# Kernel optimization log

Measured on AMD Instinct MI355X. Metric: run time of the kernel, lower is better.

The kernel has to match this reference:

```python
import jax, jax.numpy as jnp
import numpy as np

N, E, D, H = 4096, 131072, 256, 8
DH = D // H  # head dim = 32


def layer_norm(x, g, b, eps=1e-5):
    mu = jnp.mean(x, axis=-1, keepdims=True)
    var = jnp.var(x, axis=-1, keepdims=True)
    return (x - mu) * jax.lax.rsqrt(var + eps) * g + b


def mlp2(x, w1, b1, w2, b2):
    # Linear -> GELU(exact) -> Linear (dropout is identity at inference)
    return jax.nn.gelu(x @ w1 + b1, approximate=False) @ w2 + b2


def setup_inputs() -> dict:
    key = jax.random.key(0)
    ks = iter(jax.random.split(key, 32))
    s = 0.02
    d = {
        'x': jax.random.normal(next(ks), (N, D), jnp.float32),
        'edge_index': jax.random.randint(next(ks), (2, E), 0, N, jnp.int32),
        'edge_attr': jax.random.normal(next(ks), (E, D), jnp.float32),
        # GINE eps
        'eps': jnp.zeros((1,), jnp.float32),
        # edge MLP (Linear weights stored [in, out])
        'e_w1': jax.random.normal(next(ks), (D, D), jnp.float32) * s,
        'e_b1': jnp.zeros((D,), jnp.float32),
        'e_w2': jax.random.normal(next(ks), (D, D), jnp.float32) * s,
        'e_b2': jnp.zeros((D,), jnp.float32),
        # update MLP
        'u_w1': jax.random.normal(next(ks), (D, D), jnp.float32) * s,
        'u_b1': jnp.zeros((D,), jnp.float32),
        'u_w2': jax.random.normal(next(ks), (D, D), jnp.float32) * s,
        'u_b2': jnp.zeros((D,), jnp.float32),
        # LayerNorms
        'ln_local_g': jnp.ones((D,), jnp.float32), 'ln_local_b': jnp.zeros((D,), jnp.float32),
        'ln_global_g': jnp.ones((D,), jnp.float32), 'ln_global_b': jnp.zeros((D,), jnp.float32),
        'ln_ffn_g': jnp.ones((D,), jnp.float32), 'ln_ffn_b': jnp.zeros((D,), jnp.float32),
        # MHA projections ([in, out])
        'wq': jax.random.normal(next(ks), (D, D), jnp.float32) * s,
        'wk': jax.random.normal(next(ks), (D, D), jnp.float32) * s,
        'wv': jax.random.normal(next(ks), (D, D), jnp.float32) * s,
        'bq': jnp.zeros((D,), jnp.float32), 'bk': jnp.zeros((D,), jnp.float32), 'bv': jnp.zeros((D,), jnp.float32),
        'wo': jax.random.normal(next(ks), (D, D), jnp.float32) * s,
        'bo': jnp.zeros((D,), jnp.float32),
        # FFN
        'f_w1': jax.random.normal(next(ks), (D, 4 * D), jnp.float32) * s,
        'f_b1': jnp.zeros((4 * D,), jnp.float32),
        'f_w2': jax.random.normal(next(ks), (4 * D, D), jnp.float32) * s,
        'f_b2': jnp.zeros((D,), jnp.float32),
    }
    return d


def reference(x, edge_index, edge_attr, eps,
              e_w1, e_b1, e_w2, e_b2, u_w1, u_b1, u_w2, u_b2,
              ln_local_g, ln_local_b, ln_global_g, ln_global_b, ln_ffn_g, ln_ffn_b,
              wq, wk, wv, bq, bk, bv, wo, bo,
              f_w1, f_b1, f_w2, f_b2):
    src, dst = edge_index[0], edge_index[1]
    n = x.shape[0]

    # ---- local GINE conv on pre-normed features ----
    h = layer_norm(x, ln_local_g, ln_local_b)
    messages = mlp2(h[src] + edge_attr, e_w1, e_b1, e_w2, e_b2)  # [E, D]
    aggregated = jax.ops.segment_sum(messages, dst, num_segments=n)  # [N, D]
    local = mlp2((1.0 + eps) * h + aggregated, u_w1, u_b1, u_w2, u_b2)
    x = x + local

    # ---- global multihead self-attention over all nodes ----
    g = layer_norm(x, ln_global_g, ln_global_b)
    q = (g @ wq + bq).reshape(n, H, DH)
    k = (g @ wk + bk).reshape(n, H, DH)
    v = (g @ wv + bv).reshape(n, H, DH)
    scores = jnp.einsum('nhd,mhd->hnm', q, k) / jnp.sqrt(jnp.float32(DH))
    attn = jax.nn.softmax(scores, axis=-1)
    ctx = jnp.einsum('hnm,mhd->nhd', attn, v).reshape(n, D)
    x = x + (ctx @ wo + bo)

    # ---- FFN ----
    x = x + mlp2(layer_norm(x, ln_ffn_g, ln_ffn_b), f_w1, f_b1, f_w2, f_b2)
    return x
```

## Files before the change

### kernel.cpp

```cpp
#include <hip/hip_runtime.h>
#include <math.h>

#define N_NODES 4096
#define N_EDGES 131072
#define XPAD    264

using bf16x8 = __attribute__((ext_vector_type(8))) __bf16;
using bf16x4 = __attribute__((ext_vector_type(4))) __bf16;
using f32x4  = __attribute__((ext_vector_type(4))) float;
typedef unsigned short u16;

__device__ __forceinline__ u16 f2bf(float f) {
  union { __bf16 b; u16 u; } cv; cv.b = (__bf16)f; return cv.u;
}
__device__ __forceinline__ float bf2f(u16 h) {
  return __uint_as_float(((unsigned)h) << 16);
}
__device__ __forceinline__ float gelu_tanh(float x) {
  float t = x * x;
  float y = x * (1.5957691216057308f + 0.07135481627f * t);
  float e = __expf(y);
  return x - x / (1.0f + e);
}
__device__ __forceinline__ f32x4 mfma16(bf16x8 a, bf16x8 b, f32x4 c) {
  return __builtin_amdgcn_mfma_f32_16x16x32_bf16(a, b, c, 0, 0, 0);
}

struct WPtrs { const float* p[10]; };

__global__ void setup_kernel(WPtrs w, u16* __restrict__ dst, float qscale,
                             const int* __restrict__ ei, int* __restrict__ deg,
                             const float* __restrict__ bq, const float* __restrict__ bk,
                             const float* __restrict__ bv, float* __restrict__ qkvbias) {
  int blk = blockIdx.x, t = threadIdx.x;
  if (blk < 512) {
    int tid = blk * 256 + t;
    int m, ci;
    if (tid < 32768)      { m = tid >> 13;                 ci = tid & 8191; }
    else if (tid < 57344) { m = 4 + ((tid - 32768) >> 13); ci = (tid - 32768) & 8191; }
    else if (tid < 65536) { m = 7; ci = tid - 57344; }
    else if (tid < 98304) { m = 8; ci = tid - 65536; }
    else                  { m = 9; ci = tid - 98304; }
    int Cols = (m == 8) ? 1024 : 256;
    int k8   = (m == 8) ? (ci >> 10) : (ci >> 8);
    int c    = (m == 8) ? (ci & 1023) : (ci & 255);
    const float* src = w.p[m] + (size_t)(k8 * 8) * Cols + c;
    float sc = (m == 4) ? qscale : 1.0f;
    u16 tmp[8];
#pragma unroll
    for (int j = 0; j < 8; ++j) tmp[j] = f2bf(src[(size_t)j * Cols] * sc);
    size_t off;
    if (m < 4)       off = (size_t)(m << 16) + (size_t)(k8 * 256 + c) * 8;
    else if (m < 7)  off = 262144 + (size_t)(k8 * 768 + (m - 4) * 256 + c) * 8;
    else if (m == 7) off = 458752 + (size_t)(k8 * 256 + c) * 8;
    else if (m == 8) off = 524288 + (size_t)(k8 * 1024 + c) * 8;
    else             off = 786432 + (size_t)(k8 * 256 + c) * 8;
    *(uint4*)(dst + off) = *(const uint4*)tmp;
  } else if (blk < 1024) {
    int e = (blk - 512) * 256 + t;
    atomicAdd(&deg[ei[N_EDGES + e]], 1);
  } else {
#pragma unroll
    for (int i = 0; i < 3; ++i) {
      int idx = i * 256 + t;
      qkvbias[idx] = idx < 256 ? bq[idx] * qscale : (idx < 512 ? bk[idx - 256] : bv[idx - 512]);
    }
  }
}

__global__ void scan_kernel(const int* __restrict__ deg, int* __restrict__ offs) {
  __shared__ int part[1024];
  int t = threadIdx.x;
  int base = t * 4;
  int a0 = deg[base], a1 = deg[base + 1], a2 = deg[base + 2], a3 = deg[base + 3];
  int s = a0 + a1 + a2 + a3;
  part[t] = s;
  __syncthreads();
  for (int off = 1; off < 1024; off <<= 1) {
    int v = (t >= off) ? part[t - off] : 0;
    __syncthreads();
    part[t] += v;
    __syncthreads();
  }
  int excl = part[t] - s;
  offs[base] = excl;
  offs[base + 1] = excl + a0;
  offs[base + 2] = excl + a0 + a1;
  offs[base + 3] = excl + a0 + a1 + a2;
  if (t == 1023) offs[4096] = part[1023];
}

__global__ void mid_kernel(const int* __restrict__ ei, const int* __restrict__ offs,
                           int* __restrict__ cnt, int* __restrict__ eperm,
                           int* __restrict__ dst_s, int* __restrict__ src_s,
                           const float* __restrict__ x, const float* __restrict__ g,
                           const float* __restrict__ b, float* __restrict__ hf,
                           u16* __restrict__ hb) {
  int blk = blockIdx.x, t = threadIdx.x;
  if (blk < 512) {
    int e = blk * 256 + t;
    int d = ei[N_EDGES + e];
    int p = offs[d] + atomicAdd(&cnt[d], 1);
    eperm[p] = e;
    dst_s[p] = d;
    src_s[p] = ei[e];
  } else {
    int row = blk - 512;
    float v = x[(size_t)row * 256 + t];
    float s1 = v, s2 = v * v;
#pragma unroll
    for (int o = 32; o > 0; o >>= 1) { s1 += __shfl_xor(s1, o); s2 += __shfl_xor(s2, o); }
    __shared__ float a1[4], a2[4];
    int wv = t >> 6, lane = t & 63;
    if (lane == 0) { a1[wv] = s1; a2[wv] = s2; }
    __syncthreads();
    s1 = a1[0] + a1[1] + a1[2] + a1[3];
    s2 = a2[0] + a2[1] + a2[2] + a2[3];
    float mean = s1 * (1.0f / 256.0f);
    float var  = s2 * (1.0f / 256.0f) - mean * mean;
    float rs = rsqrtf(var + 1e-5f);
    float o = (v - mean) * rs * g[t] + b[t];
    hf[(size_t)row * 256 + t] = o;
    hb[(size_t)row * 256 + t] = f2bf(o);
  }
}

__launch_bounds__(256, 2)
__global__ void edge_kernel(const u16* __restrict__ hb, const float* __restrict__ ea,
                            const int* __restrict__ eperm, const int* __restrict__ src_s,
                            const int* __restrict__ dst_s,
                            const u16* __restrict__ wp1, const float* __restrict__ b1,
                            const u16* __restrict__ wp2, const float* __restrict__ b2,
                            float* __restrict__ agg) {
  __shared__ __align__(16) u16 X[128 * XPAD];
  const f32x4 fzero = {0.f, 0.f, 0.f, 0.f};
  int t = threadIdx.x;
  int lane = t & 63, wv = t >> 6;
  int lr = lane & 15, lq = lane >> 4;
  int e0 = blockIdx.x * 128;
  int col0 = wv * 64;

  const u16* b1ptr = wp1 + ((size_t)lq * 256 + col0 + lr) * 8;
  const u16* b2ptr = wp2 + ((size_t)lq * 256 + col0 + lr) * 8;
  bf16x8 bc[4], bn[4];
#pragma unroll
  for (int ct = 0; ct < 4; ++ct) bc[ct] = *(const bf16x8*)(b1ptr + ct * 128);

  int ci = (t & 31) * 8;
#pragma unroll
  for (int it = 0; it < 16; ++it) {
    int r = it * 8 + (t >> 5);
    int e = eperm[e0 + r];
    int s = src_s[e0 + r];
    const float* pa = ea + (size_t)e * 256 + ci;
    float4 a0 = *(const float4*)pa;
    float4 a1 = *(const float4*)(pa + 4);
    ushort4 h0 = *(const ushort4*)(hb + (size_t)s * 256 + ci);
    ushort4 h1 = *(const ushort4*)(hb + (size_t)s * 256 + ci + 4);
    u16 tmp[8];
    tmp[0] = f2bf(a0.x + bf2f(h0.x)); tmp[1] = f2bf(a0.y + bf2f(h0.y));
    tmp[2] = f2bf(a0.z + bf2f(h0.z)); tmp[3] = f2bf(a0.w + bf2f(h0.w));
    tmp[4] = f2bf(a1.x + bf2f(h1.x)); tmp[5] = f2bf(a1.y + bf2f(h1.y));
    tmp[6] = f2bf(a1.z + bf2f(h1.z)); tmp[7] = f2bf(a1.w + bf2f(h1.w));
    *(uint4*)&X[r * XPAD + ci] = *(const uint4*)tmp;
  }
  __syncthreads();

  f32x4 acc[8][4];
#pragma unroll
  for (int i = 0; i < 8; ++i)
#pragma unroll
    for (int j = 0; j < 4; ++j) acc[i][j] = fzero;

#pragma unroll
  for (int ks = 0; ks < 8; ++ks) {
    if (ks < 7) {
#pragma unroll
      for (int ct = 0; ct < 4; ++ct)
        bn[ct] = *(const bf16x8*)(b1ptr + (size_t)(ks + 1) * 8192 + ct * 128);
    }
    bf16x8 a[4];
#pragma unroll
    for (int rt = 0; rt < 4; ++rt)
      a[rt] = *(const bf16x8*)&X[(rt * 16 + lr) * XPAD + ks * 32 + lq * 8];
#pragma unroll
    for (int ct = 0; ct < 4; ++ct)
#pragma unroll
      for (int rt = 0; rt < 4; ++rt) acc[rt][ct] = mfma16(a[rt], bc[ct], acc[rt][ct]);
#pragma unroll
    for (int rt = 0; rt < 4; ++rt)
      a[rt] = *(const bf16x8*)&X[((rt + 4) * 16 + lr) * XPAD + ks * 32 + lq * 8];
#pragma unroll
    for (int ct = 0; ct < 4; ++ct)
#pragma unroll
      for (int rt = 0; rt < 4; ++rt) acc[rt + 4][ct] = mfma16(a[rt], bc[ct], acc[rt + 4][ct]);
#pragma unroll
    for (int ct = 0; ct < 4; ++ct) bc[ct] = bn[ct];
  }
#pragma unroll
  for (int ct = 0; ct < 4; ++ct) bn[ct] = *(const bf16x8*)(b2ptr + ct * 128);
  __syncthreads();

#pragma unroll
  for (int ct = 0; ct < 4; ++ct) {
    int c = col0 + ct * 16 + lr;
    float bb = b1[c];
#pragma unroll
    for (int rt = 0; rt < 8; ++rt)
#pragma unroll
      for (int r = 0; r < 4; ++r) {
        int row = rt * 16 + lq * 4 + r;
        X[row * XPAD + c] = f2bf(gelu_tanh(acc[rt][ct][r] + bb));
      }
  }
#pragma unroll
  for (int ct = 0; ct < 4; ++ct) bc[ct] = bn[ct];
  __syncthreads();

#pragma unroll
  for (int i = 0; i < 8; ++i)
#pragma unroll
    for (int j = 0; j < 4; ++j) acc[i][j] = fzero;
#pragma unroll
  for (int ks = 0; ks < 8; ++ks) {
    if (ks < 7) {
#pragma unroll
      for (int ct = 0; ct < 4; ++ct)
        bn[ct] = *(const bf16x8*)(b2ptr + (size_t)(ks + 1) * 8192 + ct * 128);
    }
    bf16x8 a[4];
#pragma unroll
    for (int rt = 0; rt < 4; ++rt)
      a[rt] = *(const bf16x8*)&X[(rt * 16 + lr) * XPAD + ks * 32 + lq * 8];
#pragma unroll
    for (int ct = 0; ct < 4; ++ct)
#pragma unroll
      for (int rt = 0; rt < 4; ++rt) acc[rt][ct] = mfma16(a[rt], bc[ct], acc[rt][ct]);
#pragma unroll
    for (int rt = 0; rt < 4; ++rt)
      a[rt] = *(const bf16x8*)&X[((rt + 4) * 16 + lr) * XPAD + ks * 32 + lq * 8];
#pragma unroll
    for (int ct = 0; ct < 4; ++ct)
#pragma unroll
      for (int rt = 0; rt < 4; ++rt) acc[rt + 4][ct] = mfma16(a[rt], bc[ct], acc[rt + 4][ct]);
#pragma unroll
    for (int ct = 0; ct < 4; ++ct) bc[ct] = bn[ct];
  }
  __syncthreads();

#pragma unroll
  for (int ct = 0; ct < 4; ++ct) {
    int c = col0 + ct * 16 + lr;
    float bb = b2[c];
#pragma unroll
    for (int rt = 0; rt < 8; ++rt)
#pragma unroll
      for (int r = 0; r < 4; ++r) {
        int row = rt * 16 + lq * 4 + r;
        X[row * XPAD + c] = f2bf(acc[rt][ct][r] + bb);
      }
  }
  __syncthreads();

  {
    int c4 = lane * 4;
    int rbeg = wv * 32;
    float run0 = 0.f, run1 = 0.f, run2 = 0.f, run3 = 0.f;
    int cur = dst_s[e0 + rbeg];
    for (int r = rbeg; r < rbeg + 32; ++r) {
      int d = dst_s[e0 + r];
      if (d != cur) {
        float* p = &agg[(size_t)cur * 256 + c4];
        atomicAdd(p + 0, run0); atomicAdd(p + 1, run1);
        atomicAdd(p + 2, run2); atomicAdd(p + 3, run3);
        run0 = run1 = run2 = run3 = 0.f;
        cur = d;
      }
      ushort4 xv = *(const ushort4*)&X[r * XPAD + c4];
      run0 += bf2f(xv.x); run1 += bf2f(xv.y); run2 += bf2f(xv.z); run3 += bf2f(xv.w);
    }
    float* p = &agg[(size_t)cur * 256 + c4];
    atomicAdd(p + 0, run0); atomicAdd(p + 1, run1);
    atomicAdd(p + 2, run2); atomicAdd(p + 3, run3);
  }
}

__launch_bounds__(256, 2)
__global__ void update_kernel(const float* __restrict__ hf, const float* __restrict__ agg,
                              const float* __restrict__ epsp, const float* __restrict__ xin,
                              const u16* __restrict__ wp1, const float* __restrict__ b1,
                              const u16* __restrict__ wp2, const float* __restrict__ b2,
                              const float* __restrict__ lng, const float* __restrict__ lnb,
                              float* __restrict__ x1, u16* __restrict__ gb) {
  __shared__ __align__(16) u16 X[64 * XPAD];
  __shared__ float S1[64][4], S2[64][4], MUs[64], RSs[64];
  const f32x4 fzero = {0.f, 0.f, 0.f, 0.f};
  int t = threadIdx.x;
  int lane = t & 63, wv = t >> 6;
  int lr = lane & 15, lq = lane >> 4;
  int n0 = blockIdx.x * 64;
  int col0 = wv * 64;
  float epv = 1.0f + epsp[0];
  const u16* b1ptr = wp1 + ((size_t)lq * 256 + col0 + lr) * 8;
  const u16* b2ptr = wp2 + ((size_t)lq * 256 + col0 + lr) * 8;
  bf16x8 bc[4], bn[4];
#pragma unroll
  for (int ct = 0; ct < 4; ++ct) bc[ct] = *(const bf16x8*)(b1ptr + ct * 128);
  {
    int c4 = (t & 63) * 4;
#pragma unroll
    for (int ii = 0; ii < 16; ++ii) {
      int r = ii * 4 + wv;
      float4 h = *(const float4*)(hf + (size_t)(n0 + r) * 256 + c4);
      float4 a = *(const float4*)(agg + (size_t)(n0 + r) * 256 + c4);
      *(ushort4*)&X[r * XPAD + c4] =
          make_ushort4(f2bf(epv * h.x + a.x), f2bf(epv * h.y + a.y),
                       f2bf(epv * h.z + a.z), f2bf(epv * h.w + a.w));
    }
  }
  __syncthreads();
  f32x4 acc[4][4];
#pragma unroll
  for (int i = 0; i < 4; ++i)
#pragma unroll
    for (int j = 0; j < 4; ++j) acc[i][j] = fzero;
#pragma unroll
  for (int ks = 0; ks < 8; ++ks) {
    if (ks < 7) {
#pragma unroll
      for (int ct = 0; ct < 4; ++ct)
        bn[ct] = *(const bf16x8*)(b1ptr + (size_t)(ks + 1) * 8192 + ct * 128);
    }
    bf16x8 a[4];
#pragma unroll
    for (int rt = 0; rt < 4; ++rt)
      a[rt] = *(const bf16x8*)&X[(rt * 16 + lr) * XPAD + ks * 32 + lq * 8];
#pragma unroll
    for (int ct = 0; ct < 4; ++ct)
#pragma unroll
      for (int rt = 0; rt < 4; ++rt) acc[rt][ct] = mfma16(a[rt], bc[ct], acc[rt][ct]);
#pragma unroll
    for (int ct = 0; ct < 4; ++ct) bc[ct] = bn[ct];
  }
#pragma unroll
  for (int ct = 0; ct < 4; ++ct) bn[ct] = *(const bf16x8*)(b2ptr + ct * 128);
  __syncthreads();
#pragma unroll
  for (int ct = 0; ct < 4; ++ct) {
    int c = col0 + ct * 16 + lr;
    float bb = b1[c];
#pragma unroll
    for (int rt = 0; rt < 4; ++rt)
#pragma unroll
      for (int r = 0; r < 4; ++r) {
        int row = rt * 16 + lq * 4 + r;
        X[row * XPAD + c] = f2bf(gelu_tanh(acc[rt][ct][r] + bb));
      }
  }
#pragma unroll
  for (int ct = 0; ct < 4; ++ct) bc[ct] = bn[ct];
  __syncthreads();
#pragma unroll
  for (int i = 0; i < 4; ++i)
#pragma unroll
    for (int j = 0; j < 4; ++j) acc[i][j] = fzero;
#pragma unroll
  for (int ks = 0; ks < 8; ++ks) {
    if (ks < 7) {
#pragma unroll
      for (int ct = 0; ct < 4; ++ct)
        bn[ct] = *(const bf16x8*)(b2ptr + (size_t)(ks + 1) * 8192 + ct * 128);
    }
    bf16x8 a[4];
#pragma unroll
    for (int rt = 0; rt < 4; ++rt)
      a[rt] = *(const bf16x8*)&X[(rt * 16 + lr) * XPAD + ks * 32 + lq * 8];
#pragma unroll
    for (int ct = 0; ct < 4; ++ct)
#pragma unroll
      for (int rt = 0; rt < 4; ++rt) acc[rt][ct] = mfma16(a[rt], bc[ct], acc[rt][ct]);
#pragma unroll
    for (int ct = 0; ct < 4; ++ct) bc[ct] = bn[ct];
  }
  float bb2[4];
#pragma unroll
  for (int ct = 0; ct < 4; ++ct) bb2[ct] = b2[col0 + ct * 16 + lr];
#pragma unroll
  for (int rt = 0; rt < 4; ++rt)
#pragma unroll
    for (int r = 0; r < 4; ++r) {
      int row = rt * 16 + lq * 4 + r;
      int grow = n0 + row;
      float p1 = 0.f, p2 = 0.f;
#pragma unroll
      for (int ct = 0; ct < 4; ++ct) {
        int c = col0 + ct * 16 + lr;
        float v = acc[rt][ct][r] + bb2[ct] + xin[(size_t)grow * 256 + c];
        x1[(size_t)grow * 256 + c] = v;
        acc[rt][ct][r] = v;
        p1 += v; p2 += v * v;
      }
#pragma unroll
      for (int o = 1; o < 16; o <<= 1) { p1 += __shfl_xor(p1, o); p2 += __shfl_xor(p2, o); }
      if (lr == 0) { S1[row][wv] = p1; S2[row][wv] = p2; }
    }
  __syncthreads();
  if (t < 64) {
    float s1 = S1[t][0] + S1[t][1] + S1[t][2] + S1[t][3];
    float s2 = S2[t][0] + S2[t][1] + S2[t][2] + S2[t][3];
    float mu = s1 * (1.0f / 256.0f);
    float var = s2 * (1.0f / 256.0f) - mu * mu;
    MUs[t] = mu;
    RSs[t] = rsqrtf(var + 1e-5f);
  }
  __syncthreads();
  float gv[4], bv[4];
#pragma unroll
  for (int ct = 0; ct < 4; ++ct) {
    int c = col0 + ct * 16 + lr;
    gv[ct] = lng[c]; bv[ct] = lnb[c];
  }
#pragma unroll
  for (int rt = 0; rt < 4; ++rt)
#pragma unroll
    for (int r = 0; r < 4; ++r) {
      int row = rt * 16 + lq * 4 + r;
      int grow = n0 + row;
      float mu = MUs[row], rs = RSs[row];
#pragma unroll
      for (int ct = 0; ct < 4; ++ct) {
        int c = col0 + ct * 16 + lr;
        gb[(size_t)grow * 256 + c] = f2bf((acc[rt][ct][r] - mu) * rs * gv[ct] + bv[ct]);
      }
    }
}

template <int ROWS, bool GELU_F, bool RES, bool OUTB, bool LNF>
__launch_bounds__(256, 2)
__global__ void gemm_kernel(const u16* __restrict__ A, int lda,
                            const u16* __restrict__ Wp, int K, int WCols,
                            const float* __restrict__ bias, float scale,
                            const float* __restrict__ res,
                            const float* __restrict__ lng, const float* __restrict__ lnb,
                            float* __restrict__ outf, u16* __restrict__ outh, int ldo) {
  __shared__ __align__(16) u16 X[ROWS * XPAD];
  __shared__ float S1[LNF ? ROWS : 1][4], S2[LNF ? ROWS : 1][4];
  __shared__ float MUs[LNF ? ROWS : 1], RSs[LNF ? ROWS : 1];
  constexpr int RT = ROWS / 16;
  const f32x4 fzero = {0.f, 0.f, 0.f, 0.f};
  int t = threadIdx.x;
  int lane = t & 63, wv = t >> 6;
  int lr = lane & 15, lq = lane >> 4;
  int r0 = blockIdx.x * ROWS;
  int cb = blockIdx.y * 256;
  f32x4 acc[RT][4];
#pragma unroll
  for (int i = 0; i < RT; ++i)
#pragma unroll
    for (int j = 0; j < 4; ++j) acc[i][j] = fzero;
  const u16* bptr = Wp + ((size_t)lq * WCols + cb + wv * 64 + lr) * 8;
  bf16x8 bc[4], bn[4];
#pragma unroll
  for (int ct = 0; ct < 4; ++ct) bc[ct] = *(const bf16x8*)(bptr + ct * 128);
  int rr = t >> 5, c8 = (t & 31) * 8;
  for (int kc = 0; kc < K; kc += 256) {
#pragma unroll
    for (int ii = 0; ii < ROWS / 8; ++ii) {
      int r = ii * 8 + rr;
      *(uint4*)&X[r * XPAD + c8] = *(const uint4*)(A + (size_t)(r0 + r) * lda + kc + c8);
    }
    __syncthreads();
#pragma unroll
    for (int ks = 0; ks < 8; ++ks) {
      bool more = (ks < 7) || (kc + 256 < K);
      if (more) {
        size_t koff = (ks < 7) ? ((size_t)(kc >> 3) + (ks + 1) * 4) * WCols
                               : ((size_t)((kc + 256) >> 3)) * WCols;
#pragma unroll
        for (int ct = 0; ct < 4; ++ct)
          bn[ct] = *(const bf16x8*)(bptr + (koff + ct * 16) * 8);
      }
      bf16x8 a[RT];
#pragma unroll
      for (int rt = 0; rt < RT; ++rt)
        a[rt] = *(const bf16x8*)&X[(rt * 16 + lr) * XPAD + ks * 32 + lq * 8];
#pragma unroll
      for (int ct = 0; ct < 4; ++ct)
#pragma unroll
        for (int rt = 0; rt < RT; ++rt) acc[rt][ct] = mfma16(a[rt], bc[ct], acc[rt][ct]);
#pragma unroll
      for (int ct = 0; ct < 4; ++ct) bc[ct] = bn[ct];
    }
    __syncthreads();
  }
  if (!LNF) {
#pragma unroll
    for (int ct = 0; ct < 4; ++ct) {
      int c = cb + wv * 64 + ct * 16 + lr;
      float bb = bias[c];
#pragma unroll
      for (int rt = 0; rt < RT; ++rt)
#pragma unroll
        for (int r = 0; r < 4; ++r) {
          int row = r0 + rt * 16 + lq * 4 + r;
          float v = (acc[rt][ct][r] + bb) * scale;
          if (GELU_F) v = gelu_tanh(v);
          if (RES) v += res[(size_t)row * 256 + c];
          if (OUTB) outh[(size_t)row * ldo + c] = f2bf(v);
          else      outf[(size_t)row * ldo + c] = v;
        }
    }
  } else {
    float bb[4];
#pragma unroll
    for (int ct = 0; ct < 4; ++ct) bb[ct] = bias[wv * 64 + ct * 16 + lr];
#pragma unroll
    for (int rt = 0; rt < RT; ++rt)
#pragma unroll
      for (int r = 0; r < 4; ++r) {
        int row = rt * 16 + lq * 4 + r;
        int grow = r0 + row;
        float p1 = 0.f, p2 = 0.f;
#pragma unroll
        for (int ct = 0; ct < 4; ++ct) {
          int c = wv * 64 + ct * 16 + lr;
          float v = acc[rt][ct][r] + bb[ct];
          if (RES) v += res[(size_t)grow * 256 + c];
          outf[(size_t)grow * 256 + c] = v;
          acc[rt][ct][r] = v;
          p1 += v; p2 += v * v;
        }
#pragma unroll
        for (int o = 1; o < 16; o <<= 1) { p1 += __shfl_xor(p1, o); p2 += __shfl_xor(p2, o); }
        if (lr == 0) { S1[row][wv] = p1; S2[row][wv] = p2; }
      }
    __syncthreads();
    if (t < ROWS) {
      float s1 = S1[t][0] + S1[t][1] + S1[t][2] + S1[t][3];
      float s2 = S2[t][0] + S2[t][1] + S2[t][2] + S2[t][3];
      float mu = s1 * (1.0f / 256.0f);
      float var = s2 * (1.0f / 256.0f) - mu * mu;
      MUs[t] = mu;
      RSs[t] = rsqrtf(var + 1e-5f);
    }
    __syncthreads();
    float gv[4], bv[4];
#pragma unroll
    for (int ct = 0; ct < 4; ++ct) {
      int c = wv * 64 + ct * 16 + lr;
      gv[ct] = lng[c]; bv[ct] = lnb[c];
    }
#pragma unroll
    for (int rt = 0; rt < RT; ++rt)
#pragma unroll
      for (int r = 0; r < 4; ++r) {
        int row = rt * 16 + lq * 4 + r;
        int grow = r0 + row;
        float mu = MUs[row], rs = RSs[row];
#pragma unroll
        for (int ct = 0; ct < 4; ++ct) {
          int c = wv * 64 + ct * 16 + lr;
          outh[(size_t)grow * ldo + c] = f2bf((acc[rt][ct][r] - mu) * rs * gv[ct] + bv[ct]);
        }
      }
  }
}

__launch_bounds__(256, 4)
__global__ void attn_kernel(const u16* __restrict__ qkv, u16* __restrict__ ctx) {
  __shared__ u16 Kt[128 * 40];
  __shared__ u16 Vt[32 * 136];
  __shared__ u16 P[4][16 * 136];
  const f32x4 fzero = {0.f, 0.f, 0.f, 0.f};
  int t = threadIdx.x;
  int lane = t & 63, wv = t >> 6;
  int lr = lane & 15, lq = lane >> 4;
  int head = blockIdx.y;
  int q0 = blockIdx.x * 64 + wv * 16;
  const u16* qb = qkv;
  const u16* kb = qkv + 256;
  const u16* vb = qkv + 512;
  bf16x8 qf = *(const bf16x8*)(qb + (size_t)(q0 + lr) * 768 + head * 32 + lq * 8);
  f32x4 o0 = fzero, o1 = fzero;
  float l_i[4] = {0.f, 0.f, 0.f, 0.f};
  int key2 = t >> 1, khalf = (t & 1) * 16;
  int vd = t >> 4, vkb = (t & 15) * 8;
  for (int k0 = 0; k0 < N_NODES; k0 += 128) {
    const u16* kpg = kb + (size_t)(k0 + key2) * 768 + head * 32 + khalf;
    *(uint4*)&Kt[key2 * 40 + khalf]     = *(const uint4*)kpg;
    *(uint4*)&Kt[key2 * 40 + khalf + 8] = *(const uint4*)(kpg + 8);
#pragma unroll
    for (int dd = 0; dd < 2; ++dd) {
      int d = vd + dd * 16;
      u16 tv[8];
#pragma unroll
      for (int j = 0; j < 8; ++j)
        tv[j] = vb[(size_t)(k0 + vkb + j) * 768 + head * 32 + d];
      *(uint4*)&Vt[d * 136 + vkb] = *(const uint4*)tv;
    }
    __syncthreads();
    f32x4 s[8];
#pragma unroll
    for (int ct = 0; ct < 8; ++ct) {
      bf16x8 bk = *(const bf16x8*)&Kt[(ct * 16 + lr) * 40 + lq * 8];
      s[ct] = mfma16(qf, bk, fzero);
    }
#pragma unroll
    for (int ct = 0; ct < 8; ++ct)
#pragma unroll
      for (int r = 0; r < 4; ++r) s[ct][r] = __expf(s[ct][r]);
#pragma unroll
    for (int r = 0; r < 4; ++r) {
      float ps = ((s[0][r] + s[1][r]) + (s[2][r] + s[3][r])) +
                 ((s[4][r] + s[5][r]) + (s[6][r] + s[7][r]));
#pragma unroll
      for (int d = 1; d < 16; d <<= 1) ps += __shfl_xor(ps, d);
      l_i[r] += ps;
    }
#pragma unroll
    for (int ct = 0; ct < 8; ++ct)
#pragma unroll
      for (int r = 0; r < 4; ++r)
        P[wv][(lq * 4 + r) * 136 + ct * 16 + lr] = f2bf(s[ct][r]);
#pragma unroll
    for (int kp = 0; kp < 4; ++kp) {
      bf16x8 pa = *(const bf16x8*)&P[wv][lr * 136 + kp * 32 + lq * 8];
      bf16x8 v0 = *(const bf16x8*)&Vt[lr * 136 + kp * 32 + lq * 8];
      bf16x8 v1 = *(const bf16x8*)&Vt[(16 + lr) * 136 + kp * 32 + lq * 8];
      o0 = mfma16(pa, v0, o0);
      o1 = mfma16(pa, v1, o1);
    }
    __syncthreads();
  }
#pragma unroll
  for (int r = 0; r < 4; ++r) {
    float inv = 1.0f / l_i[r];
    int row = q0 + lq * 4 + r;
    ctx[(size_t)row * 256 + head * 32 + lr]      = f2bf(o0[r] * inv);
    ctx[(size_t)row * 256 + head * 32 + 16 + lr] = f2bf(o1[r] * inv);
  }
}

extern "C" void kernel_launch(void* const* d_in, const int* in_sizes, int n_in,
                              void* d_out, int out_size, void* d_ws, size_t ws_size,
                              hipStream_t stream) {
  const float* x         = (const float*)d_in[0];
  const int*   ei        = (const int*)d_in[1];
  const float* edge_attr = (const float*)d_in[2];
  const float* eps       = (const float*)d_in[3];
  const float* e_w1 = (const float*)d_in[4];
  const float* e_b1 = (const float*)d_in[5];
  const float* e_w2 = (const float*)d_in[6];
  const float* e_b2 = (const float*)d_in[7];
  const float* u_w1 = (const float*)d_in[8];
  const float* u_b1 = (const float*)d_in[9];
  const float* u_w2 = (const float*)d_in[10];
  const float* u_b2 = (const float*)d_in[11];
  const float* ln_local_g  = (const float*)d_in[12];
  const float* ln_local_b  = (const float*)d_in[13];
  const float* ln_global_g = (const float*)d_in[14];
  const float* ln_global_b = (const float*)d_in[15];
  const float* ln_ffn_g    = (const float*)d_in[16];
  const float* ln_ffn_b    = (const float*)d_in[17];
  const float* wq = (const float*)d_in[18];
  const float* wk = (const float*)d_in[19];
  const float* wv = (const float*)d_in[20];
  const float* bq = (const float*)d_in[21];
  const float* bk = (const float*)d_in[22];
  const float* bv = (const float*)d_in[23];
  const float* wo = (const float*)d_in[24];
  const float* bo = (const float*)d_in[25];
  const float* f_w1 = (const float*)d_in[26];
  const float* f_b1 = (const float*)d_in[27];
  const float* f_w2 = (const float*)d_in[28];
  const float* f_b2 = (const float*)d_in[29];

  char* ws = (char*)d_ws;
  u16*   WP      = (u16*)(ws + 0);
  float* agg     = (float*)(ws + (2u  << 20));
  int*   deg     = (int*)(ws + (6u  << 20));
  int*   cnt     = (int*)(ws + (6u  << 20) + (16u << 10));
  int*   offs    = (int*)(ws + (6u  << 20) + (32u << 10));
  float* qkvbias = (float*)(ws + (6u << 20) + (64u << 10));
  float* hf      = (float*)(ws + (7u  << 20));
  float* x1      = (float*)(ws + (11u << 20));
  u16*   gb      = (u16*)(ws + (15u << 20));
  u16*   qkvb_   = (u16*)(ws + (17u << 20));
  u16*   ctxb    = (u16*)(ws + (23u << 20));
  float* x2      = (float*)(ws + (25u << 20));
  u16*   yb      = (u16*)(ws + (29u << 20));
  u16*   hid     = (u16*)(ws + (31u << 20));
  int*   eperm   = (int*)(ws + (39u << 20));
  int*   dst_s   = (int*)(ws + (39u << 20) + (512u << 10));
  int*   src_s   = (int*)(ws + (40u << 20));
  u16*   hb      = (u16*)(ws + (40u << 20) + (512u << 10));

  const size_t O_EW1 = 0, O_EW2 = 65536, O_UW1 = 131072, O_UW2 = 196608,
               O_QKV = 262144, O_WO = 458752, O_FW1 = 524288, O_FW2 = 786432;
  const float qscale = 0.17677669529663687f;

  hipMemsetAsync(agg, 0, (4u << 20) + (32u << 10), stream);

  WPtrs wp;
  wp.p[0] = e_w1; wp.p[1] = e_w2; wp.p[2] = u_w1; wp.p[3] = u_w2;
  wp.p[4] = wq;   wp.p[5] = wk;   wp.p[6] = wv;   wp.p[7] = wo;
  wp.p[8] = f_w1; wp.p[9] = f_w2;
  setup_kernel<<<1025, 256, 0, stream>>>(wp, WP, qscale, ei, deg, bq, bk, bv, qkvbias);
  scan_kernel<<<1, 1024, 0, stream>>>(deg, offs);
  mid_kernel<<<4608, 256, 0, stream>>>(ei, offs, cnt, eperm, dst_s, src_s,
                                       x, ln_local_g, ln_local_b, hf, hb);

  edge_kernel<<<N_EDGES / 128, 256, 0, stream>>>(hb, edge_attr, eperm, src_s, dst_s,
                                                 WP + O_EW1, e_b1, WP + O_EW2, e_b2, agg);

  update_kernel<<<N_NODES / 64, 256, 0, stream>>>(hf, agg, eps, x,
                                                  WP + O_UW1, u_b1, WP + O_UW2, u_b2,
                                                  ln_global_g, ln_global_b, x1, gb);

  gemm_kernel<64, false, false, true, false><<<dim3(64, 3), 256, 0, stream>>>(
      gb, 256, WP + O_QKV, 256, 768, qkvbias, 1.0f, nullptr, nullptr, nullptr,
      nullptr, qkvb_, 768);

  attn_kernel<<<dim3(64, 8), 256, 0, stream>>>(qkvb_, ctxb);

  gemm_kernel<32, false, true, false, true><<<dim3(128, 1), 256, 0, stream>>>(
      ctxb, 256, WP + O_WO, 256, 256, bo, 1.0f, x1, ln_ffn_g, ln_ffn_b, x2, yb, 256);

  gemm_kernel<64, true, false, true, false><<<dim3(64, 4), 256, 0, stream>>>(
      yb, 256, WP + O_FW1, 256, 1024, f_b1, 1.0f, nullptr, nullptr, nullptr,
      nullptr, hid, 1024);

  gemm_kernel<32, false, true, false, false><<<dim3(128, 1), 256, 0, stream>>>(
      hid, 1024, WP + O_FW2, 1024, 256, f_b2, 1.0f, x2, nullptr, nullptr,
      (float*)d_out, nullptr, 256);
}
```

Measured before the change: 550.2 us.

## Split QKV output into separate Q, K and transposed V buffers for attention

The QKV GEMM epilogue now writes Q and K into separate row-major buffers and V transposed (feature-major), so the attention kernel can load V tiles with vector loads instead of strided scalar gathers. The attention kernel uses 64-key tiles with smaller shared memory, targets higher occupancy through launch bounds, and stores probabilities as fp32 in an XOR-swizzled shared buffer before converting to bf16. The transposed V store in the GEMM epilogue is uncoalesced, and the smaller tiles double the number of loop iterations and barriers. XPAD also changes from 264 to 272.

```diff
diff --git a/kernel.cpp b/kernel.cpp
--- a/kernel.cpp
+++ b/kernel.cpp
@@ -3,10 +3,9 @@
 
 #define N_NODES 4096
 #define N_EDGES 131072
-#define XPAD    264
+#define XPAD    272
 
 using bf16x8 = __attribute__((ext_vector_type(8))) __bf16;
-using bf16x4 = __attribute__((ext_vector_type(4))) __bf16;
 using f32x4  = __attribute__((ext_vector_type(4))) float;
 typedef unsigned short u16;
 
@@ -435,14 +434,15 @@
     }
 }
 
-template <int ROWS, bool GELU_F, bool RES, bool OUTB, bool LNF>
+template <int ROWS, bool GELU_F, bool RES, bool OUTB, bool LNF, bool QKV>
 __launch_bounds__(256, 2)
 __global__ void gemm_kernel(const u16* __restrict__ A, int lda,
                             const u16* __restrict__ Wp, int K, int WCols,
                             const float* __restrict__ bias, float scale,
                             const float* __restrict__ res,
                             const float* __restrict__ lng, const float* __restrict__ lnb,
-                            float* __restrict__ outf, u16* __restrict__ outh, int ldo) {
+                            float* __restrict__ outf, u16* __restrict__ outh,
+                            u16* __restrict__ outh2, u16* __restrict__ vtp, int ldo) {
   __shared__ __align__(16) u16 X[ROWS * XPAD];
   __shared__ float S1[LNF ? ROWS : 1][4], S2[LNF ? ROWS : 1][4];
   __shared__ float MUs[LNF ? ROWS : 1], RSs[LNF ? ROWS : 1];
@@ -493,7 +493,24 @@
     }
     __syncthreads();
   }
-  if (!LNF) {
+  if (QKV) {
+    int y = blockIdx.y;
+#pragma unroll
+    for (int ct = 0; ct < 4; ++ct) {
+      int c = cb + wv * 64 + ct * 16 + lr;
+      float bb = bias[c];
+#pragma unroll
+      for (int rt = 0; rt < RT; ++rt)
+#pragma unroll
+        for (int r = 0; r < 4; ++r) {
+          int row = r0 + rt * 16 + lq * 4 + r;
+          u16 hv = f2bf(acc[rt][ct][r] + bb);
+          if (y == 0)      outh[(size_t)row * 256 + c] = hv;
+          else if (y == 1) outh2[(size_t)row * 256 + (c - 256)] = hv;
+          else             vtp[(size_t)(c - 512) * 4096 + row] = hv;
+        }
+    }
+  } else if (!LNF) {
 #pragma unroll
     for (int ct = 0; ct < 4; ++ct) {
       int c = cb + wv * 64 + ct * 16 + lr;
@@ -566,67 +583,64 @@
   }
 }
 
-__launch_bounds__(256, 4)
-__global__ void attn_kernel(const u16* __restrict__ qkv, u16* __restrict__ ctx) {
-  __shared__ u16 Kt[128 * 40];
-  __shared__ u16 Vt[32 * 136];
-  __shared__ u16 P[4][16 * 136];
+__launch_bounds__(256, 6)
+__global__ void attn_kernel(const u16* __restrict__ qb, const u16* __restrict__ kb,
+                            const u16* __restrict__ vT, u16* __restrict__ ctx) {
+  __shared__ u16 Kt[64 * 40];
+  __shared__ u16 Vt[32 * 72];
+  __shared__ float P32[4][1024];
   const f32x4 fzero = {0.f, 0.f, 0.f, 0.f};
   int t = threadIdx.x;
   int lane = t & 63, wv = t >> 6;
   int lr = lane & 15, lq = lane >> 4;
   int head = blockIdx.y;
   int q0 = blockIdx.x * 64 + wv * 16;
-  const u16* qb = qkv;
-  const u16* kb = qkv + 256;
-  const u16* vb = qkv + 512;
-  bf16x8 qf = *(const bf16x8*)(qb + (size_t)(q0 + lr) * 768 + head * 32 + lq * 8);
+  bf16x8 qf = *(const bf16x8*)(qb + (size_t)(q0 + lr) * 256 + head * 32 + lq * 8);
   f32x4 o0 = fzero, o1 = fzero;
   float l_i[4] = {0.f, 0.f, 0.f, 0.f};
-  int key2 = t >> 1, khalf = (t & 1) * 16;
-  int vd = t >> 4, vkb = (t & 15) * 8;
-  for (int k0 = 0; k0 < N_NODES; k0 += 128) {
-    const u16* kpg = kb + (size_t)(k0 + key2) * 768 + head * 32 + khalf;
-    *(uint4*)&Kt[key2 * 40 + khalf]     = *(const uint4*)kpg;
-    *(uint4*)&Kt[key2 * 40 + khalf + 8] = *(const uint4*)(kpg + 8);
-#pragma unroll
-    for (int dd = 0; dd < 2; ++dd) {
-      int d = vd + dd * 16;
-      u16 tv[8];
-#pragma unroll
-      for (int j = 0; j < 8; ++j)
-        tv[j] = vb[(size_t)(k0 + vkb + j) * 768 + head * 32 + d];
-      *(uint4*)&Vt[d * 136 + vkb] = *(const uint4*)tv;
-    }
-    __syncthreads();
-    f32x4 s[8];
-#pragma unroll
-    for (int ct = 0; ct < 8; ++ct) {
+  int kkey = t >> 2, kdp = (t & 3) * 8;
+  int vd = t >> 3, vkc = (t & 7) * 8;
+  const u16* vbase = vT + (size_t)(head * 32 + vd) * 4096;
+  int psw = (lr >> 2) & 3;
+  float* pw = &P32[wv][0];
+  for (int k0 = 0; k0 < N_NODES; k0 += 64) {
+    *(uint4*)&Kt[kkey * 40 + kdp] = *(const uint4*)(kb + (size_t)(k0 + kkey) * 256 + head * 32 + kdp);
+    *(uint4*)&Vt[vd * 72 + vkc]   = *(const uint4*)(vbase + k0 + vkc);
+    __syncthreads();
+    f32x4 s[4];
+#pragma unroll
+    for (int ct = 0; ct < 4; ++ct) {
       bf16x8 bk = *(const bf16x8*)&Kt[(ct * 16 + lr) * 40 + lq * 8];
       s[ct] = mfma16(qf, bk, fzero);
     }
 #pragma unroll
-    for (int ct = 0; ct < 8; ++ct)
+    for (int ct = 0; ct < 4; ++ct)
 #pragma unroll
       for (int r = 0; r < 4; ++r) s[ct][r] = __expf(s[ct][r]);
 #pragma unroll
     for (int r = 0; r < 4; ++r) {
-      float ps = ((s[0][r] + s[1][r]) + (s[2][r] + s[3][r])) +
-                 ((s[4][r] + s[5][r]) + (s[6][r] + s[7][r]));
+      float ps = (s[0][r] + s[1][r]) + (s[2][r] + s[3][r]);
 #pragma unroll
       for (int d = 1; d < 16; d <<= 1) ps += __shfl_xor(ps, d);
       l_i[r] += ps;
     }
 #pragma unroll
-    for (int ct = 0; ct < 8; ++ct)
-#pragma unroll
-      for (int r = 0; r < 4; ++r)
-        P[wv][(lq * 4 + r) * 136 + ct * 16 + lr] = f2bf(s[ct][r]);
-#pragma unroll
-    for (int kp = 0; kp < 4; ++kp) {
-      bf16x8 pa = *(const bf16x8*)&P[wv][lr * 136 + kp * 32 + lq * 8];
-      bf16x8 v0 = *(const bf16x8*)&Vt[lr * 136 + kp * 32 + lq * 8];
-      bf16x8 v1 = *(const bf16x8*)&Vt[(16 + lr) * 136 + kp * 32 + lq * 8];
+    for (int ct = 0; ct < 4; ++ct) {
+      int col = ct * 16 + lr;
+      int w = (((col >> 2) ^ lq) << 2) + (col & 3);
+#pragma unroll
+      for (int r = 0; r < 4; ++r) pw[(lq * 4 + r) * 64 + w] = s[ct][r];
+    }
+#pragma unroll
+    for (int kp = 0; kp < 2; ++kp) {
+      int cch = kp * 8 + lq * 2;
+      f32x4 f0 = *(const f32x4*)&pw[lr * 64 + ((cch ^ psw) << 2)];
+      f32x4 f1 = *(const f32x4*)&pw[lr * 64 + (((cch + 1) ^ psw) << 2)];
+      bf16x8 pa;
+#pragma unroll
+      for (int j = 0; j < 4; ++j) { pa[j] = (__bf16)f0[j]; pa[j + 4] = (__bf16)f1[j]; }
+      bf16x8 v0 = *(const bf16x8*)&Vt[lr * 72 + kp * 32 + lq * 8];
+      bf16x8 v1 = *(const bf16x8*)&Vt[(16 + lr) * 72 + kp * 32 + lq * 8];
       o0 = mfma16(pa, v0, o0);
       o1 = mfma16(pa, v1, o1);
     }
@@ -685,7 +699,9 @@
   float* hf      = (float*)(ws + (7u  << 20));
   float* x1      = (float*)(ws + (11u << 20));
   u16*   gb      = (u16*)(ws + (15u << 20));
-  u16*   qkvb_   = (u16*)(ws + (17u << 20));
+  u16*   qbuf    = (u16*)(ws + (17u << 20));
+  u16*   kbuf    = (u16*)(ws + (19u << 20));
+  u16*   vTb     = (u16*)(ws + (21u << 20));
   u16*   ctxb    = (u16*)(ws + (23u << 20));
   float* x2      = (float*)(ws + (25u << 20));
   u16*   yb      = (u16*)(ws + (29u << 20));
@@ -717,20 +733,21 @@
                                                   WP + O_UW1, u_b1, WP + O_UW2, u_b2,
                                                   ln_global_g, ln_global_b, x1, gb);
 
-  gemm_kernel<64, false, false, true, false><<<dim3(64, 3), 256, 0, stream>>>(
+  gemm_kernel<64, false, false, true, false, true><<<dim3(64, 3), 256, 0, stream>>>(
       gb, 256, WP + O_QKV, 256, 768, qkvbias, 1.0f, nullptr, nullptr, nullptr,
-      nullptr, qkvb_, 768);
-
-  attn_kernel<<<dim3(64, 8), 256, 0, stream>>>(qkvb_, ctxb);
-
-  gemm_kernel<32, false, true, false, true><<<dim3(128, 1), 256, 0, stream>>>(
-      ctxb, 256, WP + O_WO, 256, 256, bo, 1.0f, x1, ln_ffn_g, ln_ffn_b, x2, yb, 256);
-
-  gemm_kernel<64, true, false, true, false><<<dim3(64, 4), 256, 0, stream>>>(
+      nullptr, qbuf, kbuf, vTb, 256);
+
+  attn_kernel<<<dim3(64, 8), 256, 0, stream>>>(qbuf, kbuf, vTb, ctxb);
+
+  gemm_kernel<32, false, true, false, true, false><<<dim3(128, 1), 256, 0, stream>>>(
+      ctxb, 256, WP + O_WO, 256, 256, bo, 1.0f, x1, ln_ffn_g, ln_ffn_b, x2, yb,
+      nullptr, nullptr, 256);
+
+  gemm_kernel<64, true, false, true, false, false><<<dim3(64, 4), 256, 0, stream>>>(
       yb, 256, WP + O_FW1, 256, 1024, f_b1, 1.0f, nullptr, nullptr, nullptr,
-      nullptr, hid, 1024);
-
-  gemm_kernel<32, false, true, false, false><<<dim3(128, 1), 256, 0, stream>>>(
+      nullptr, hid, nullptr, nullptr, 1024);
+
+  gemm_kernel<32, false, true, false, false, false><<<dim3(128, 1), 256, 0, stream>>>(
       hid, 1024, WP + O_FW2, 1024, 256, f_b2, 1.0f, x2, nullptr, nullptr,
-      (float*)d_out, nullptr, 256);
-}
+      (float*)d_out, nullptr, nullptr, nullptr, 256);
+}
```

Result: no change. 541.7 us (-1.5%).
